# Kernel tuning notes

Measured on AMD Instinct MI355X. Metric: run time of the kernel, lower is better.

Reference implementation:

```python
import jax, jax.numpy as jnp
import numpy as np


def _ln(x, g, b, eps=1e-5):
    m = x.mean(-1, keepdims=True)
    v = ((x - m) ** 2).mean(-1, keepdims=True)
    return (x - m) * jax.lax.rsqrt(v + eps) * g + b


def setup_inputs() -> dict:
    key = jax.random.key(0)
    ks = jax.random.split(key, 16)
    B, C, D, H, W = 1, 192, 8, 32, 32
    nh, k, hid = 6, 7, 768
    n = lambda i, shape: jax.random.normal(ks[i], shape, dtype=jnp.float32) * 0.02
    return {
        'x': jax.random.normal(ks[0], (B, C, D, H, W), dtype=jnp.float32),
        'pos_emb': n(1, (1, D, C)),
        't_ln1_g': jnp.ones((C,), jnp.float32), 't_ln1_b': jnp.zeros((C,), jnp.float32),
        't_qkv_w': n(2, (C, 3 * C)),
        't_out_w': n(3, (C, C)), 't_out_b': jnp.zeros((C,), jnp.float32),
        't_ln2_g': jnp.ones((C,), jnp.float32), 't_ln2_b': jnp.zeros((C,), jnp.float32),
        't_fc1_w': n(4, (C, hid)), 't_fc1_b': jnp.zeros((hid,), jnp.float32),
        't_fc2_w': n(5, (hid, C)), 't_fc2_b': jnp.zeros((C,), jnp.float32),
        't_lnf_g': jnp.ones((C,), jnp.float32), 't_lnf_b': jnp.zeros((C,), jnp.float32),
        's_ln1_g': jnp.ones((C,), jnp.float32), 's_ln1_b': jnp.zeros((C,), jnp.float32),
        's_qkv_w': n(6, (C, 3 * C)), 's_qkv_b': jnp.zeros((3 * C,), jnp.float32),
        's_rpb': n(7, (nh, 2 * k - 1, 2 * k - 1)),
        's_proj_w': n(8, (C, C)), 's_proj_b': jnp.zeros((C,), jnp.float32),
        's_ln2_g': jnp.ones((C,), jnp.float32), 's_ln2_b': jnp.zeros((C,), jnp.float32),
        's_fc1_w': n(9, (C, hid)), 's_fc1_b': jnp.zeros((hid,), jnp.float32),
        's_fc2_w': n(10, (hid, C)), 's_fc2_b': jnp.zeros((C,), jnp.float32),
    }


def reference(x, pos_emb, t_ln1_g, t_ln1_b, t_qkv_w, t_out_w, t_out_b,
              t_ln2_g, t_ln2_b, t_fc1_w, t_fc1_b, t_fc2_w, t_fc2_b,
              t_lnf_g, t_lnf_b, s_ln1_g, s_ln1_b, s_qkv_w, s_qkv_b, s_rpb,
              s_proj_w, s_proj_b, s_ln2_g, s_ln2_b, s_fc1_w, s_fc1_b,
              s_fc2_w, s_fc2_b):
    B, C, D, H, W = x.shape
    nh = 6
    d = C // nh
    k = 7
    scale = d ** -0.5

    # ---- Time transformer: attend over the D frames per spatial position ----
    t = jnp.transpose(x, (0, 3, 4, 2, 1)).reshape(B * H * W, D, C)  # (b h w) s c
    t = t + pos_emb
    y = _ln(t, t_ln1_g, t_ln1_b)
    qkv = (y @ t_qkv_w).reshape(-1, D, 3, nh, d)
    q, kk, v = [jnp.transpose(qkv[:, :, i], (0, 2, 1, 3)) for i in range(3)]  # [N,nh,D,d]
    att = jax.nn.softmax(jnp.einsum('nhid,nhjd->nhij', q, kk) * scale, axis=-1)
    o = jnp.einsum('nhij,nhjd->nhid', att, v)
    o = jnp.transpose(o, (0, 2, 1, 3)).reshape(-1, D, C)
    t = t + (o @ t_out_w + t_out_b)
    y = _ln(t, t_ln2_g, t_ln2_b)
    t = t + (jax.nn.gelu(y @ t_fc1_w + t_fc1_b, approximate=False) @ t_fc2_w + t_fc2_b)
    t = _ln(t, t_lnf_g, t_lnf_b)
    x = x + jnp.transpose(t.reshape(B, H, W, D, C), (0, 4, 3, 1, 2))

    # ---- Space transformer: neighborhood (NAT) attention per frame ----
    s = jnp.transpose(x, (0, 2, 3, 4, 1)).reshape(B * D, H, W, C)  # (b s) h w c
    shortcut = s
    y = _ln(s, s_ln1_g, s_ln1_b)
    qkv = (y @ s_qkv_w + s_qkv_b).reshape(B * D, H, W, 3, nh, d)
    qkv = jnp.transpose(qkv, (3, 0, 4, 1, 2, 5))  # [3,N,nh,H,W,d]
    q, kk, v = qkv[0] * scale, qkv[1], qkv[2]
    half = k // 2
    sh = jnp.clip(jnp.arange(H) - half, 0, H - k)   # window start per row (edge-clamped)
    sw = jnp.clip(jnp.arange(W) - half, 0, W - k)
    idx_h = sh[:, None] + jnp.arange(k)             # [H,k] neighbor rows
    idx_w = sw[:, None] + jnp.arange(k)             # [W,k] neighbor cols
    rel_h = idx_h - jnp.arange(H)[:, None] + (k - 1)  # rel-pos-bias indices in [0,2k-2]
    rel_w = idx_w - jnp.arange(W)[:, None] + (k - 1)
    Kn = kk[:, :, idx_h][:, :, :, :, idx_w]  # [N,nh,H,k,W,k,d]
    Vn = v[:, :, idx_h][:, :, :, :, idx_w]
    att = jnp.einsum('nehwd,nehawbd->nehwab', q, Kn)  # [N,nh,H,W,k,k]
    bias = jnp.transpose(s_rpb[:, rel_h][:, :, :, rel_w], (0, 1, 3, 2, 4))  # [nh,H,W,k,k]
    att = att + bias[None]
    shp = att.shape
    att = jax.nn.softmax(att.reshape(shp[0], shp[1], shp[2], shp[3], k * k), axis=-1).reshape(shp)
    o = jnp.einsum('nehwab,nehawbd->nehwd', att, Vn)
    o = jnp.transpose(o, (0, 2, 3, 1, 4)).reshape(B * D, H, W, C)
    s = shortcut + (o @ s_proj_w + s_proj_b)
    y = _ln(s, s_ln2_g, s_ln2_b)
    s = s + (jax.nn.gelu(y @ s_fc1_w + s_fc1_b, approximate=False) @ s_fc2_w + s_fc2_b)
    x_space = jnp.transpose(s.reshape(B, D, H, W, C), (0, 4, 1, 2, 3))
    return x + x_space
```

## Files before the change

kernel.cpp:

```cpp
#include <hip/hip_runtime.h>
#include <hip/hip_bf16.h>
#include <math.h>

typedef __hip_bfloat16 bf16;
typedef short bf16x8 __attribute__((ext_vector_type(8)));
typedef float f32x4 __attribute__((ext_vector_type(4)));

__device__ __forceinline__ float b2f(bf16 v) { return __bfloat162float(v); }
__device__ __forceinline__ bf16 f2b(float v) { return __float2bfloat16(v); }
__device__ __forceinline__ float us2f(unsigned short u) {
  return __uint_as_float(((unsigned)u) << 16);
}
__device__ __forceinline__ unsigned short f2us(float f) {
  bf16 h = __float2bfloat16(f);
  return *reinterpret_cast<unsigned short*>(&h);
}
__device__ __forceinline__ float ldin(const void* p, size_t i, int f32) {
  return f32 ? ((const float*)p)[i] : b2f(((const bf16*)p)[i]);
}

#define CC 192
#define DD 8
#define HH 32
#define WW 32
#define NHEAD 6
#define HDIM 32
#define HID 768
#define NTOK 8192
#define ATT_SCALE 0.17677669529663687f

__global__ void probe_dtype_kernel(const unsigned short* __restrict__ xu,
                                   int* __restrict__ flag) {
  int lane = threadIdx.x;
  int insane = 0;
  for (int i = lane; i < 256; i += 64) {
    float a = fabsf(us2f(xu[i]));
    bool sane = (a == 0.0f) || (a > 9.5e-7f && a < 64.0f);
    if (!sane) insane++;
  }
  for (int off = 32; off; off >>= 1) insane += __shfl_xor(insane, off);
  if (lane == 0) *flag = (insane > 32) ? 1 : 0;
}

__global__ void wconv_kernel(const void* w0, const void* w1, const void* w2,
                             const void* w3, const void* w4, const void* w5,
                             const void* w6, const void* w7,
                             bf16* __restrict__ WT, const int* __restrict__ dfl) {
  int f32 = *dfl;
  int idx = blockIdx.x * 256 + threadIdx.x;
  if (idx >= 884736) return;
  const void* src; int K, N, loc;
  if      (idx < 110592) { src = w0; K = 192; N = 576; loc = idx; }
  else if (idx < 147456) { src = w1; K = 192; N = 192; loc = idx - 110592; }
  else if (idx < 294912) { src = w2; K = 192; N = 768; loc = idx - 147456; }
  else if (idx < 442368) { src = w3; K = 768; N = 192; loc = idx - 294912; }
  else if (idx < 552960) { src = w4; K = 192; N = 576; loc = idx - 442368; }
  else if (idx < 589824) { src = w5; K = 192; N = 192; loc = idx - 552960; }
  else if (idx < 737280) { src = w6; K = 192; N = 768; loc = idx - 589824; }
  else                   { src = w7; K = 768; N = 192; loc = idx - 737280; }
  int n = loc / K, k = loc - n * K;
  WT[idx] = f2b(ldin(src, (size_t)k * N + n, f32));
}

#define WOFF_TQKV  0
#define WOFF_TOUT  110592
#define WOFF_TFC1  147456
#define WOFF_TFC2  294912
#define WOFF_SQKV  442368
#define WOFF_SPROJ 552960
#define WOFF_SFC1  589824
#define WOFF_SFC2  737280

__global__ void build_ln1_kernel(const void* __restrict__ x, const void* __restrict__ pos,
                                 const void* __restrict__ g, const void* __restrict__ b,
                                 float* __restrict__ T, bf16* __restrict__ Y,
                                 const int* __restrict__ dfl) {
  int f32 = *dfl;
  int wave = (blockIdx.x * blockDim.x + threadIdx.x) >> 6;
  int lane = threadIdx.x & 63;
  if (wave >= NTOK) return;
  int d = wave & 7, hw = wave >> 3;
  float v[3];
#pragma unroll
  for (int e = 0; e < 3; e++) {
    int c = lane + e * 64;
    v[e] = ldin(x, (size_t)((c << 3) + d) * 1024 + hw, f32) +
           ldin(pos, (size_t)d * CC + c, f32);
  }
  float* tr = T + (size_t)wave * CC;
#pragma unroll
  for (int e = 0; e < 3; e++) tr[lane + e * 64] = v[e];
  float s = v[0] + v[1] + v[2];
  for (int off = 32; off; off >>= 1) s += __shfl_xor(s, off);
  float mean = s * (1.0f / CC);
  float d0 = v[0] - mean, d1 = v[1] - mean, d2 = v[2] - mean;
  float q = d0 * d0 + d1 * d1 + d2 * d2;
  for (int off = 32; off; off >>= 1) q += __shfl_xor(q, off);
  float rstd = rsqrtf(q * (1.0f / CC) + 1e-5f);
  bf16* o = Y + (size_t)wave * CC;
  o[lane]       = f2b(d0 * rstd * ldin(g, lane, f32)       + ldin(b, lane, f32));
  o[lane + 64]  = f2b(d1 * rstd * ldin(g, lane + 64, f32)  + ldin(b, lane + 64, f32));
  o[lane + 128] = f2b(d2 * rstd * ldin(g, lane + 128, f32) + ldin(b, lane + 128, f32));
}

__global__ void ln_kernel(const float* __restrict__ in, bf16* __restrict__ out,
                          const void* __restrict__ g, const void* __restrict__ b,
                          int rows, const int* __restrict__ dfl) {
  int f32 = *dfl;
  int wave = (blockIdx.x * blockDim.x + threadIdx.x) >> 6;
  int lane = threadIdx.x & 63;
  if (wave >= rows) return;
  const float* r = in + (size_t)wave * CC;
  float v0 = r[lane], v1 = r[lane + 64], v2 = r[lane + 128];
  float s = v0 + v1 + v2;
  for (int off = 32; off; off >>= 1) s += __shfl_xor(s, off);
  float mean = s * (1.0f / CC);
  float d0 = v0 - mean, d1 = v1 - mean, d2 = v2 - mean;
  float q = d0 * d0 + d1 * d1 + d2 * d2;
  for (int off = 32; off; off >>= 1) q += __shfl_xor(q, off);
  float rstd = rsqrtf(q * (1.0f / CC) + 1e-5f);
  bf16* o = out + (size_t)wave * CC;
  o[lane]       = f2b(d0 * rstd * ldin(g, lane, f32)       + ldin(b, lane, f32));
  o[lane + 64]  = f2b(d1 * rstd * ldin(g, lane + 64, f32)  + ldin(b, lane + 64, f32));
  o[lane + 128] = f2b(d2 * rstd * ldin(g, lane + 128, f32) + ldin(b, lane + 128, f32));
}

template <int TM, bool BIAS, bool GELU, bool RES, bool OUTBF, bool FINAL>
__global__ void gemm_kernel(const bf16* __restrict__ A, const bf16* __restrict__ WT,
                            const void* __restrict__ bias, const float* __restrict__ R,
                            void* __restrict__ Cout, const float* __restrict__ X2,
                            int M, int N, int K, const int* __restrict__ dfl) {
  int f32 = *dfl;
  __shared__ __align__(16) unsigned short As[TM * 64 * 72];
  __shared__ __align__(16) unsigned short Bs[64 * 72];
  int bm = blockIdx.y * (TM * 64), bn = blockIdx.x * 64;
  int tid = threadIdx.x;
  int w = tid >> 6;
  int lane = tid & 63;
  int lm = lane & 15;
  int lk = lane >> 4;

  f32x4 acc[TM][4];
#pragma unroll
  for (int i = 0; i < TM; i++)
#pragma unroll
    for (int j = 0; j < 4; j++) acc[i][j] = (f32x4){0.f, 0.f, 0.f, 0.f};

  const unsigned short* Au = reinterpret_cast<const unsigned short*>(A);
  const unsigned short* Wu = reinterpret_cast<const unsigned short*>(WT);

  for (int k0 = 0; k0 < K; k0 += 64) {
#pragma unroll
    for (int u = 0; u < TM * 2; u++) {
      int unit = tid + u * 256;
      int row = unit >> 3, seg = unit & 7;
      uint4 v = *reinterpret_cast<const uint4*>(
          &Au[(size_t)(bm + row) * K + k0 + seg * 8]);
      *reinterpret_cast<uint4*>(&As[row * 72 + seg * 8]) = v;
    }
#pragma unroll
    for (int u = 0; u < 2; u++) {
      int unit = tid + u * 256;
      int n = unit >> 3, seg = unit & 7;
      uint4 v = *reinterpret_cast<const uint4*>(
          &Wu[(size_t)(bn + n) * K + k0 + seg * 8]);
      *reinterpret_cast<uint4*>(&Bs[n * 72 + seg * 8]) = v;
    }
    __syncthreads();

#pragma unroll
    for (int kc = 0; kc < 2; kc++) {
      bf16x8 af[TM], bfr[4];
#pragma unroll
      for (int tm = 0; tm < TM; tm++)
        af[tm] = *reinterpret_cast<const bf16x8*>(
            &As[(w * (TM * 16) + tm * 16 + lm) * 72 + kc * 32 + lk * 8]);
#pragma unroll
      for (int tn = 0; tn < 4; tn++)
        bfr[tn] = *reinterpret_cast<const bf16x8*>(
            &Bs[(tn * 16 + lm) * 72 + kc * 32 + lk * 8]);
#pragma unroll
      for (int tm = 0; tm < TM; tm++)
#pragma unroll
        for (int tn = 0; tn < 4; tn++)
          acc[tm][tn] = __builtin_amdgcn_mfma_f32_16x16x32_bf16(
              af[tm], bfr[tn], acc[tm][tn], 0, 0, 0);
    }
    __syncthreads();
  }

#pragma unroll
  for (int tn = 0; tn < 4; tn++) {
    int col = bn + tn * 16 + lm;
    float bv = BIAS ? ldin(bias, col, f32) : 0.f;
#pragma unroll
    for (int tm = 0; tm < TM; tm++) {
      int row0 = bm + w * (TM * 16) + tm * 16 + lk * 4;
#pragma unroll
      for (int r = 0; r < 4; r++) {
        int row = row0 + r;
        float v = acc[tm][tn][r];
        if (BIAS) v += bv;
        if (GELU) v = 0.5f * v * (1.0f + erff(v * 0.70710678118654752f));
        size_t idx = (size_t)row * N + col;
        if (RES) v += R[idx];
        if (FINAL) {
          float o = v + X2[(size_t)row * CC + col];
          if (f32) ((float*)Cout)[(size_t)col * NTOK + row] = o;
          else     ((bf16*)Cout)[(size_t)col * NTOK + row] = f2b(o);
        } else if (OUTBF) {
          ((bf16*)Cout)[idx] = f2b(v);
        } else {
          ((float*)Cout)[idx] = v;
        }
      }
    }
  }
}

__global__ void time_attn_kernel(const bf16* __restrict__ qkv, bf16* __restrict__ O) {
  __shared__ float q[NHEAD][DD][HDIM];
  __shared__ float k[NHEAD][DD][HDIM];
  __shared__ float v[NHEAD][DD][HDIM];
  __shared__ float p[NHEAD][DD][DD];
  int n = blockIdx.x;
  int head = threadIdx.x >> 5;
  int dd = threadIdx.x & 31;
  for (int s = 0; s < DD; s++) {
    const bf16* row = qkv + (size_t)(n * DD + s) * (3 * CC);
    q[head][s][dd] = b2f(row[head * HDIM + dd]);
    k[head][s][dd] = b2f(row[CC + head * HDIM + dd]);
    v[head][s][dd] = b2f(row[2 * CC + head * HDIM + dd]);
  }
  __syncthreads();
  for (int pair = dd; pair < 64; pair += 32) {
    int sq = pair >> 3, sk = pair & 7;
    float sum = 0.f;
#pragma unroll
    for (int e = 0; e < HDIM; e++) sum += q[head][sq][e] * k[head][sk][e];
    p[head][sq][sk] = sum * ATT_SCALE;
  }
  __syncthreads();
  if (dd < DD) {
    float mx = -1e30f;
    for (int sk = 0; sk < DD; sk++) mx = fmaxf(mx, p[head][dd][sk]);
    float sum = 0.f;
    for (int sk = 0; sk < DD; sk++) { float e = expf(p[head][dd][sk] - mx); p[head][dd][sk] = e; sum += e; }
    float inv = 1.0f / sum;
    for (int sk = 0; sk < DD; sk++) p[head][dd][sk] *= inv;
  }
  __syncthreads();
  for (int sq = 0; sq < DD; sq++) {
    float sum = 0.f;
#pragma unroll
    for (int sk = 0; sk < DD; sk++) sum += p[head][sq][sk] * v[head][sk][dd];
    O[(size_t)(n * DD + sq) * CC + head * HDIM + dd] = f2b(sum);
  }
}

__global__ void epi_ln1_kernel(const float* __restrict__ T, const void* __restrict__ x,
                               const void* __restrict__ gf, const void* __restrict__ bf,
                               const void* __restrict__ g1, const void* __restrict__ b1,
                               float* __restrict__ X1T, bf16* __restrict__ Y,
                               const int* __restrict__ dfl) {
  int f32 = *dfl;
  int wave = (blockIdx.x * blockDim.x + threadIdx.x) >> 6;
  int lane = threadIdx.x & 63;
  if (wave >= NTOK) return;
  const float* r = T + (size_t)wave * CC;
  float v0 = r[lane], v1 = r[lane + 64], v2 = r[lane + 128];
  float s = v0 + v1 + v2;
  for (int off = 32; off; off >>= 1) s += __shfl_xor(s, off);
  float mean = s * (1.0f / CC);
  float d0 = v0 - mean, d1 = v1 - mean, d2 = v2 - mean;
  float q = d0 * d0 + d1 * d1 + d2 * d2;
  for (int off = 32; off; off >>= 1) q += __shfl_xor(q, off);
  float rstd = rsqrtf(q * (1.0f / CC) + 1e-5f);
  int d = wave & 7, hw = wave >> 3;
  int m = d * 1024 + hw;
  float xv[3];
#pragma unroll
  for (int e = 0; e < 3; e++) {
    int c = lane + e * 64;
    float dv = (e == 0 ? d0 : (e == 1 ? d1 : d2));
    float normed = dv * rstd * ldin(gf, c, f32) + ldin(bf, c, f32);
    xv[e] = ldin(x, (size_t)((c << 3) + d) * 1024 + hw, f32) + normed;
  }
  float* o = X1T + (size_t)m * CC;
#pragma unroll
  for (int e = 0; e < 3; e++) o[lane + e * 64] = xv[e];
  float s2 = xv[0] + xv[1] + xv[2];
  for (int off = 32; off; off >>= 1) s2 += __shfl_xor(s2, off);
  float mean2 = s2 * (1.0f / CC);
  float e0 = xv[0] - mean2, e1 = xv[1] - mean2, e2 = xv[2] - mean2;
  float q2 = e0 * e0 + e1 * e1 + e2 * e2;
  for (int off = 32; off; off >>= 1) q2 += __shfl_xor(q2, off);
  float rstd2 = rsqrtf(q2 * (1.0f / CC) + 1e-5f);
  bf16* y = Y + (size_t)m * CC;
  y[lane]       = f2b(e0 * rstd2 * ldin(g1, lane, f32)       + ldin(b1, lane, f32));
  y[lane + 64]  = f2b(e1 * rstd2 * ldin(g1, lane + 64, f32)  + ldin(b1, lane + 64, f32));
  y[lane + 128] = f2b(e2 * rstd2 * ldin(g1, lane + 128, f32) + ldin(b1, lane + 128, f32));
}

#define NKEY 224
#define PKS 40
#define PVS 232
__global__ void nat_attn_kernel(const bf16* __restrict__ qkv, const void* __restrict__ rpb,
                                bf16* __restrict__ O, const int* __restrict__ dfl) {
  int f32 = *dfl;
  __shared__ __align__(16) unsigned short Ks[NKEY * PKS];
  __shared__ __align__(16) unsigned short Vs[32 * PVS];
  __shared__ __align__(16) unsigned short Qs[64 * PKS];
  __shared__ __align__(16) unsigned short Ps[64 * PVS];
  __shared__ float rb[176];

  int blk = blockIdx.x;
  int frame = blk & 7;
  int rest = blk >> 3;
  int h = rest % 6;
  int tile = rest / 6;
  int ty = tile >> 2, tx = tile & 3;
  int base_h = min(max(ty * 8 - 3, 0), HH - 7);
  int base_w = min(max(tx * 8 - 3, 0), WW - 7);

  int tid = threadIdx.x;

  for (int i = tid; i < 169; i += 256) rb[i] = ldin(rpb, (size_t)h * 169 + i, f32);
  for (int u = tid; u < 784; u += 256) {
    int j = u >> 2, seg = u & 3;
    int a = j / 14, bb = j - a * 14;
    int ih = min(base_h + a, HH - 1), iw = min(base_w + bb, WW - 1);
    int mg = frame * 1024 + ih * 32 + iw;
    uint4 v = *reinterpret_cast<const uint4*>(qkv + (size_t)mg * 576 + 192 + h * 32 + seg * 8);
    *reinterpret_cast<uint4*>(&Ks[j * PKS + seg * 8]) = v;
  }
  for (int u = tid; u < 784; u += 256) {
    int j = u >> 2, seg = u & 3;
    int a = j / 14, bb = j - a * 14;
    int ih = min(base_h + a, HH - 1), iw = min(base_w + bb, WW - 1);
    int mg = frame * 1024 + ih * 32 + iw;
    uint4 v = *reinterpret_cast<const uint4*>(qkv + (size_t)mg * 576 + 384 + h * 32 + seg * 8);
    unsigned arr[4] = {v.x, v.y, v.z, v.w};
#pragma unroll
    for (int e = 0; e < 4; e++) {
      Vs[(seg * 8 + e * 2) * PVS + j]     = (unsigned short)(arr[e] & 0xffffu);
      Vs[(seg * 8 + e * 2 + 1) * PVS + j] = (unsigned short)(arr[e] >> 16);
    }
  }
  for (int u = tid; u < 32 * (PVS - 196); u += 256) {
    int dd = u / (PVS - 196), c = 196 + u % (PVS - 196);
    Vs[dd * PVS + c] = 0;
  }
  {
    int q = tid >> 2, seg = tid & 3;
    int qy = ty * 8 + (q >> 3), qx = tx * 8 + (q & 7);
    int mg = frame * 1024 + qy * 32 + qx;
    uint4 v = *reinterpret_cast<const uint4*>(qkv + (size_t)mg * 576 + h * 32 + seg * 8);
    *reinterpret_cast<uint4*>(&Qs[q * PKS + seg * 8]) = v;
  }
  __syncthreads();

  int w = tid >> 6;
  int lane = tid & 63;
  int c = lane & 15;
  int lk = lane >> 4;

  bf16x8 aq = *reinterpret_cast<const bf16x8*>(&Qs[(w * 16 + c) * PKS + lk * 8]);
  f32x4 sc[14];
#pragma unroll
  for (int f = 0; f < 14; f++) {
    bf16x8 bk = *reinterpret_cast<const bf16x8*>(&Ks[(f * 16 + c) * PKS + lk * 8]);
    sc[f] = __builtin_amdgcn_mfma_f32_16x16x32_bf16(aq, bk, (f32x4){0.f, 0.f, 0.f, 0.f}, 0, 0, 0);
  }

#pragma unroll
  for (int f = 0; f < 14; f++) {
    int key = f * 16 + c;
    int a = key / 14, bb = key - a * 14;
    int ih = base_h + a, iw = base_w + bb;
    bool keyok = key < 196;
#pragma unroll
    for (int r = 0; r < 4; r++) {
      int qloc = w * 16 + lk * 4 + r;
      int qy = ty * 8 + (qloc >> 3), qx = tx * 8 + (qloc & 7);
      int sh = min(max(qy - 3, 0), HH - 7);
      int sw = min(max(qx - 3, 0), WW - 7);
      bool valid = keyok && ((unsigned)(ih - sh) < 7u) && ((unsigned)(iw - sw) < 7u);
      int bidx = valid ? (ih - qy + 6) * 13 + (iw - qx + 6) : 0;
      float s = sc[f][r] * ATT_SCALE + rb[bidx];
      sc[f][r] = valid ? s : -1e30f;
    }
  }

  float sm[4];
#pragma unroll
  for (int r = 0; r < 4; r++) {
    float m = sc[0][r];
#pragma unroll
    for (int f = 1; f < 14; f++) m = fmaxf(m, sc[f][r]);
    for (int off = 8; off; off >>= 1) m = fmaxf(m, __shfl_xor(m, off));
    float s = 0.f;
#pragma unroll
    for (int f = 0; f < 14; f++) { float e = __expf(sc[f][r] - m); sc[f][r] = e; s += e; }
    for (int off = 8; off; off >>= 1) s += __shfl_xor(s, off);
    sm[r] = 1.0f / s;
  }
#pragma unroll
  for (int f = 0; f < 14; f++)
#pragma unroll
    for (int r = 0; r < 4; r++)
      Ps[(w * 16 + lk * 4 + r) * PVS + f * 16 + c] = f2us(sc[f][r] * sm[r]);
  __syncthreads();

  f32x4 oacc[2] = {(f32x4){0.f, 0.f, 0.f, 0.f}, (f32x4){0.f, 0.f, 0.f, 0.f}};
#pragma unroll
  for (int kt = 0; kt < 7; kt++) {
    bf16x8 ap = *reinterpret_cast<const bf16x8*>(&Ps[(w * 16 + c) * PVS + kt * 32 + lk * 8]);
#pragma unroll
    for (int dt = 0; dt < 2; dt++) {
      bf16x8 bv = *reinterpret_cast<const bf16x8*>(&Vs[(dt * 16 + c) * PVS + kt * 32 + lk * 8]);
      oacc[dt] = __builtin_amdgcn_mfma_f32_16x16x32_bf16(ap, bv, oacc[dt], 0, 0, 0);
    }
  }

#pragma unroll
  for (int dt = 0; dt < 2; dt++)
#pragma unroll
    for (int r = 0; r < 4; r++) {
      int qloc = w * 16 + lk * 4 + r;
      int qy = ty * 8 + (qloc >> 3), qx = tx * 8 + (qloc & 7);
      int mg = frame * 1024 + qy * 32 + qx;
      O[(size_t)mg * CC + h * 32 + dt * 16 + c] = f2b(oacc[dt][r]);
    }
}

extern "C" void kernel_launch(void* const* d_in, const int* in_sizes, int n_in,
                              void* d_out, int out_size, void* d_ws, size_t ws_size,
                              hipStream_t stream) {
  const void* x        = d_in[0];
  const void* pos_emb  = d_in[1];
  const void* t_ln1_g  = d_in[2];
  const void* t_ln1_b  = d_in[3];
  const void* t_qkv_w  = d_in[4];
  const void* t_out_w  = d_in[5];
  const void* t_out_b  = d_in[6];
  const void* t_ln2_g  = d_in[7];
  const void* t_ln2_b  = d_in[8];
  const void* t_fc1_w  = d_in[9];
  const void* t_fc1_b  = d_in[10];
  const void* t_fc2_w  = d_in[11];
  const void* t_fc2_b  = d_in[12];
  const void* t_lnf_g  = d_in[13];
  const void* t_lnf_b  = d_in[14];
  const void* s_ln1_g  = d_in[15];
  const void* s_ln1_b  = d_in[16];
  const void* s_qkv_w  = d_in[17];
  const void* s_qkv_b  = d_in[18];
  const void* s_rpb    = d_in[19];
  const void* s_proj_w = d_in[20];
  const void* s_proj_b = d_in[21];
  const void* s_ln2_g  = d_in[22];
  const void* s_ln2_b  = d_in[23];
  const void* s_fc1_w  = d_in[24];
  const void* s_fc1_b  = d_in[25];
  const void* s_fc2_w  = d_in[26];
  const void* s_fc2_b  = d_in[27];

  float* ws = (float*)d_ws;
  const size_t SZ = (size_t)NTOK * CC;
  const size_t need = (5 * SZ + 4 + 442368 + 16) * sizeof(float);
  if (ws_size < need) return;

  float* T   = ws;
  float* X1T = ws + SZ;
  bf16*  Y   = (bf16*)(ws + 2 * SZ);
  bf16*  O   = (bf16*)(ws + 2 * SZ + SZ / 2);
  bf16*  QKV = (bf16*)(ws + 3 * SZ);
  bf16*  Hb  = QKV;
  float* S   = T;
  int*   dfl = (int*)(ws + 5 * SZ);
  bf16*  WT  = (bf16*)(ws + 5 * SZ + 4);

  dim3 blk256(256);

  probe_dtype_kernel<<<1, 64, 0, stream>>>((const unsigned short*)x, dfl);
  wconv_kernel<<<3456, blk256, 0, stream>>>(
      t_qkv_w, t_out_w, t_fc1_w, t_fc2_w, s_qkv_w, s_proj_w, s_fc1_w, s_fc2_w, WT, dfl);

  build_ln1_kernel<<<NTOK / 4, blk256, 0, stream>>>(x, pos_emb, t_ln1_g, t_ln1_b, T, Y, dfl);
  gemm_kernel<2, false, false, false, true, false><<<dim3(9, 64), blk256, 0, stream>>>(
      Y, WT + WOFF_TQKV, nullptr, nullptr, QKV, nullptr, NTOK, 3 * CC, CC, dfl);
  time_attn_kernel<<<1024, 192, 0, stream>>>(QKV, O);
  gemm_kernel<1, true, false, true, false, false><<<dim3(3, 128), blk256, 0, stream>>>(
      O, WT + WOFF_TOUT, t_out_b, T, T, nullptr, NTOK, CC, CC, dfl);
  ln_kernel<<<NTOK / 4, blk256, 0, stream>>>(T, Y, t_ln2_g, t_ln2_b, NTOK, dfl);
  gemm_kernel<2, true, true, false, true, false><<<dim3(12, 64), blk256, 0, stream>>>(
      Y, WT + WOFF_TFC1, t_fc1_b, nullptr, Hb, nullptr, NTOK, HID, CC, dfl);
  gemm_kernel<1, true, false, true, false, false><<<dim3(3, 128), blk256, 0, stream>>>(
      Hb, WT + WOFF_TFC2, t_fc2_b, T, T, nullptr, NTOK, CC, HID, dfl);
  epi_ln1_kernel<<<NTOK / 4, blk256, 0, stream>>>(
      T, x, t_lnf_g, t_lnf_b, s_ln1_g, s_ln1_b, X1T, Y, dfl);

  gemm_kernel<2, true, false, false, true, false><<<dim3(9, 64), blk256, 0, stream>>>(
      Y, WT + WOFF_SQKV, s_qkv_b, nullptr, QKV, nullptr, NTOK, 3 * CC, CC, dfl);
  nat_attn_kernel<<<768, blk256, 0, stream>>>(QKV, s_rpb, O, dfl);
  gemm_kernel<1, true, false, true, false, false><<<dim3(3, 128), blk256, 0, stream>>>(
      O, WT + WOFF_SPROJ, s_proj_b, X1T, S, nullptr, NTOK, CC, CC, dfl);
  ln_kernel<<<NTOK / 4, blk256, 0, stream>>>(S, Y, s_ln2_g, s_ln2_b, NTOK, dfl);
  gemm_kernel<2, true, true, false, true, false><<<dim3(12, 64), blk256, 0, stream>>>(
      Y, WT + WOFF_SFC1, s_fc1_b, nullptr, Hb, nullptr, NTOK, HID, CC, dfl);
  gemm_kernel<1, true, false, true, false, true><<<dim3(3, 128), blk256, 0, stream>>>(
      Hb, WT + WOFF_SFC2, s_fc2_b, S, d_out, X1T, NTOK, CC, HID, dfl);
}
```

Baseline: 279.7 us.

## Fuse N=192 GEMMs with following LayerNorm and merge dtype probe into weight conversion

```diff
diff --git a/kernel.cpp b/kernel.cpp
--- a/kernel.cpp
+++ b/kernel.cpp
@@ -29,24 +29,22 @@
 #define NTOK 8192
 #define ATT_SCALE 0.17677669529663687f
 
-__global__ void probe_dtype_kernel(const unsigned short* __restrict__ xu,
-                                   int* __restrict__ flag) {
-  int lane = threadIdx.x;
-  int insane = 0;
-  for (int i = lane; i < 256; i += 64) {
-    float a = fabsf(us2f(xu[i]));
-    bool sane = (a == 0.0f) || (a > 9.5e-7f && a < 64.0f);
-    if (!sane) insane++;
-  }
-  for (int off = 32; off; off >>= 1) insane += __shfl_xor(insane, off);
-  if (lane == 0) *flag = (insane > 32) ? 1 : 0;
-}
-
-__global__ void wconv_kernel(const void* w0, const void* w1, const void* w2,
+__global__ void wconv_kernel(const unsigned short* __restrict__ xu,
+                             const void* w0, const void* w1, const void* w2,
                              const void* w3, const void* w4, const void* w5,
                              const void* w6, const void* w7,
-                             bf16* __restrict__ WT, const int* __restrict__ dfl) {
-  int f32 = *dfl;
+                             bf16* __restrict__ WT, int* __restrict__ flag) {
+  __shared__ int cnt[4];
+  {
+    float a = fabsf(us2f(xu[threadIdx.x]));
+    bool insane = !((a == 0.0f) || (a > 9.5e-7f && a < 64.0f));
+    unsigned long long mask = __ballot(insane);
+    if ((threadIdx.x & 63) == 0) cnt[threadIdx.x >> 6] = __popcll(mask);
+  }
+  __syncthreads();
+  int f32 = (cnt[0] + cnt[1] + cnt[2] + cnt[3]) > 32;
+  if (blockIdx.x == 0 && threadIdx.x == 0) *flag = f32;
+
   int idx = blockIdx.x * 256 + threadIdx.x;
   if (idx >= 884736) return;
   const void* src; int K, N, loc;
@@ -98,28 +96,6 @@
   for (int off = 32; off; off >>= 1) q += __shfl_xor(q, off);
   float rstd = rsqrtf(q * (1.0f / CC) + 1e-5f);
   bf16* o = Y + (size_t)wave * CC;
-  o[lane]       = f2b(d0 * rstd * ldin(g, lane, f32)       + ldin(b, lane, f32));
-  o[lane + 64]  = f2b(d1 * rstd * ldin(g, lane + 64, f32)  + ldin(b, lane + 64, f32));
-  o[lane + 128] = f2b(d2 * rstd * ldin(g, lane + 128, f32) + ldin(b, lane + 128, f32));
-}
-
-__global__ void ln_kernel(const float* __restrict__ in, bf16* __restrict__ out,
-                          const void* __restrict__ g, const void* __restrict__ b,
-                          int rows, const int* __restrict__ dfl) {
-  int f32 = *dfl;
-  int wave = (blockIdx.x * blockDim.x + threadIdx.x) >> 6;
-  int lane = threadIdx.x & 63;
-  if (wave >= rows) return;
-  const float* r = in + (size_t)wave * CC;
-  float v0 = r[lane], v1 = r[lane + 64], v2 = r[lane + 128];
-  float s = v0 + v1 + v2;
-  for (int off = 32; off; off >>= 1) s += __shfl_xor(s, off);
-  float mean = s * (1.0f / CC);
-  float d0 = v0 - mean, d1 = v1 - mean, d2 = v2 - mean;
-  float q = d0 * d0 + d1 * d1 + d2 * d2;
-  for (int off = 32; off; off >>= 1) q += __shfl_xor(q, off);
-  float rstd = rsqrtf(q * (1.0f / CC) + 1e-5f);
-  bf16* o = out + (size_t)wave * CC;
   o[lane]       = f2b(d0 * rstd * ldin(g, lane, f32)       + ldin(b, lane, f32));
   o[lane + 64]  = f2b(d1 * rstd * ldin(g, lane + 64, f32)  + ldin(b, lane + 64, f32));
   o[lane + 128] = f2b(d2 * rstd * ldin(g, lane + 128, f32) + ldin(b, lane + 128, f32));
@@ -218,6 +194,126 @@
   }
 }
 
+template <bool EPI>
+__global__ void gemm_ln_kernel(const bf16* __restrict__ A, const bf16* __restrict__ WT,
+                               const void* __restrict__ bias, const float* __restrict__ R,
+                               const void* __restrict__ x,
+                               const void* __restrict__ g0, const void* __restrict__ b0,
+                               const void* __restrict__ g1, const void* __restrict__ b1,
+                               float* __restrict__ Fout, bf16* __restrict__ Yout,
+                               int K, const int* __restrict__ dfl) {
+  int f32 = *dfl;
+  __shared__ __align__(16) unsigned short As[64 * 72];
+  __shared__ __align__(16) unsigned short Bs[192 * 72];
+  int bm = blockIdx.x * 64;
+  int tid = threadIdx.x;
+  int w = tid >> 6;
+  int lane = tid & 63;
+  int lm = lane & 15;
+  int lk = lane >> 4;
+
+  f32x4 acc[12];
+#pragma unroll
+  for (int j = 0; j < 12; j++) acc[j] = (f32x4){0.f, 0.f, 0.f, 0.f};
+
+  const unsigned short* Au = reinterpret_cast<const unsigned short*>(A);
+  const unsigned short* Wu = reinterpret_cast<const unsigned short*>(WT);
+
+  for (int k0 = 0; k0 < K; k0 += 64) {
+#pragma unroll
+    for (int u = 0; u < 2; u++) {
+      int unit = tid + u * 256;
+      int row = unit >> 3, seg = unit & 7;
+      uint4 v = *reinterpret_cast<const uint4*>(
+          &Au[(size_t)(bm + row) * K + k0 + seg * 8]);
+      *reinterpret_cast<uint4*>(&As[row * 72 + seg * 8]) = v;
+    }
+#pragma unroll
+    for (int u = 0; u < 6; u++) {
+      int unit = tid + u * 256;
+      int n = unit >> 3, seg = unit & 7;
+      uint4 v = *reinterpret_cast<const uint4*>(
+          &Wu[(size_t)n * K + k0 + seg * 8]);
+      *reinterpret_cast<uint4*>(&Bs[n * 72 + seg * 8]) = v;
+    }
+    __syncthreads();
+
+#pragma unroll
+    for (int kc = 0; kc < 2; kc++) {
+      bf16x8 af = *reinterpret_cast<const bf16x8*>(
+          &As[(w * 16 + lm) * 72 + kc * 32 + lk * 8]);
+#pragma unroll
+      for (int tn = 0; tn < 12; tn++) {
+        bf16x8 bfr = *reinterpret_cast<const bf16x8*>(
+            &Bs[(tn * 16 + lm) * 72 + kc * 32 + lk * 8]);
+        acc[tn] = __builtin_amdgcn_mfma_f32_16x16x32_bf16(af, bfr, acc[tn], 0, 0, 0);
+      }
+    }
+    __syncthreads();
+  }
+
+  float bv[12];
+#pragma unroll
+  for (int tn = 0; tn < 12; tn++) bv[tn] = ldin(bias, tn * 16 + lm, f32);
+
+#pragma unroll
+  for (int r = 0; r < 4; r++) {
+    int row = bm + w * 16 + lk * 4 + r;
+    float v[12];
+    float s = 0.f;
+#pragma unroll
+    for (int tn = 0; tn < 12; tn++) {
+      float t = acc[tn][r] + bv[tn] + R[(size_t)row * CC + tn * 16 + lm];
+      v[tn] = t;
+      s += t;
+    }
+    for (int off = 1; off < 16; off <<= 1) s += __shfl_xor(s, off);
+    float mean = s * (1.0f / CC);
+    float q = 0.f;
+#pragma unroll
+    for (int tn = 0; tn < 12; tn++) { float d = v[tn] - mean; q += d * d; }
+    for (int off = 1; off < 16; off <<= 1) q += __shfl_xor(q, off);
+    float rstd = rsqrtf(q * (1.0f / CC) + 1e-5f);
+
+    if (!EPI) {
+#pragma unroll
+      for (int tn = 0; tn < 12; tn++) {
+        int col = tn * 16 + lm;
+        Fout[(size_t)row * CC + col] = v[tn];
+        Yout[(size_t)row * CC + col] =
+            f2b((v[tn] - mean) * rstd * ldin(g0, col, f32) + ldin(b0, col, f32));
+      }
+    } else {
+      int d = row & 7, hw = row >> 3;
+      int m = d * 1024 + hw;
+      float xv[12];
+      float s2 = 0.f;
+#pragma unroll
+      for (int tn = 0; tn < 12; tn++) {
+        int col = tn * 16 + lm;
+        float normed = (v[tn] - mean) * rstd * ldin(g0, col, f32) + ldin(b0, col, f32);
+        float t = ldin(x, (size_t)((col << 3) + d) * 1024 + hw, f32) + normed;
+        xv[tn] = t;
+        s2 += t;
+        Fout[(size_t)m * CC + col] = t;
+      }
+      for (int off = 1; off < 16; off <<= 1) s2 += __shfl_xor(s2, off);
+      float mean2 = s2 * (1.0f / CC);
+      float q2 = 0.f;
+#pragma unroll
+      for (int tn = 0; tn < 12; tn++) { float dd = xv[tn] - mean2; q2 += dd * dd; }
+      for (int off = 1; off < 16; off <<= 1) q2 += __shfl_xor(q2, off);
+      float rstd2 = rsqrtf(q2 * (1.0f / CC) + 1e-5f);
+#pragma unroll
+      for (int tn = 0; tn < 12; tn++) {
+        int col = tn * 16 + lm;
+        Yout[(size_t)m * CC + col] =
+            f2b((xv[tn] - mean2) * rstd2 * ldin(g1, col, f32) + ldin(b1, col, f32));
+      }
+    }
+  }
+}
+
 __global__ void time_attn_kernel(const bf16* __restrict__ qkv, bf16* __restrict__ O) {
   __shared__ float q[NHEAD][DD][HDIM];
   __shared__ float k[NHEAD][DD][HDIM];
@@ -256,50 +352,6 @@
     for (int sk = 0; sk < DD; sk++) sum += p[head][sq][sk] * v[head][sk][dd];
     O[(size_t)(n * DD + sq) * CC + head * HDIM + dd] = f2b(sum);
   }
-}
-
-__global__ void epi_ln1_kernel(const float* __restrict__ T, const void* __restrict__ x,
-                               const void* __restrict__ gf, const void* __restrict__ bf,
-                               const void* __restrict__ g1, const void* __restrict__ b1,
-                               float* __restrict__ X1T, bf16* __restrict__ Y,
-                               const int* __restrict__ dfl) {
-  int f32 = *dfl;
-  int wave = (blockIdx.x * blockDim.x + threadIdx.x) >> 6;
-  int lane = threadIdx.x & 63;
-  if (wave >= NTOK) return;
-  const float* r = T + (size_t)wave * CC;
-  float v0 = r[lane], v1 = r[lane + 64], v2 = r[lane + 128];
-  float s = v0 + v1 + v2;
-  for (int off = 32; off; off >>= 1) s += __shfl_xor(s, off);
-  float mean = s * (1.0f / CC);
-  float d0 = v0 - mean, d1 = v1 - mean, d2 = v2 - mean;
-  float q = d0 * d0 + d1 * d1 + d2 * d2;
-  for (int off = 32; off; off >>= 1) q += __shfl_xor(q, off);
-  float rstd = rsqrtf(q * (1.0f / CC) + 1e-5f);
-  int d = wave & 7, hw = wave >> 3;
-  int m = d * 1024 + hw;
-  float xv[3];
-#pragma unroll
-  for (int e = 0; e < 3; e++) {
-    int c = lane + e * 64;
-    float dv = (e == 0 ? d0 : (e == 1 ? d1 : d2));
-    float normed = dv * rstd * ldin(gf, c, f32) + ldin(bf, c, f32);
-    xv[e] = ldin(x, (size_t)((c << 3) + d) * 1024 + hw, f32) + normed;
-  }
-  float* o = X1T + (size_t)m * CC;
-#pragma unroll
-  for (int e = 0; e < 3; e++) o[lane + e * 64] = xv[e];
-  float s2 = xv[0] + xv[1] + xv[2];
-  for (int off = 32; off; off >>= 1) s2 += __shfl_xor(s2, off);
-  float mean2 = s2 * (1.0f / CC);
-  float e0 = xv[0] - mean2, e1 = xv[1] - mean2, e2 = xv[2] - mean2;
-  float q2 = e0 * e0 + e1 * e1 + e2 * e2;
-  for (int off = 32; off; off >>= 1) q2 += __shfl_xor(q2, off);
-  float rstd2 = rsqrtf(q2 * (1.0f / CC) + 1e-5f);
-  bf16* y = Y + (size_t)m * CC;
-  y[lane]       = f2b(e0 * rstd2 * ldin(g1, lane, f32)       + ldin(b1, lane, f32));
-  y[lane + 64]  = f2b(e1 * rstd2 * ldin(g1, lane + 64, f32)  + ldin(b1, lane + 64, f32));
-  y[lane + 128] = f2b(e2 * rstd2 * ldin(g1, lane + 128, f32) + ldin(b1, lane + 128, f32));
 }
 
 #define NKEY 224
@@ -483,30 +535,29 @@
 
   dim3 blk256(256);
 
-  probe_dtype_kernel<<<1, 64, 0, stream>>>((const unsigned short*)x, dfl);
   wconv_kernel<<<3456, blk256, 0, stream>>>(
+      (const unsigned short*)x,
       t_qkv_w, t_out_w, t_fc1_w, t_fc2_w, s_qkv_w, s_proj_w, s_fc1_w, s_fc2_w, WT, dfl);
 
   build_ln1_kernel<<<NTOK / 4, blk256, 0, stream>>>(x, pos_emb, t_ln1_g, t_ln1_b, T, Y, dfl);
   gemm_kernel<2, false, false, false, true, false><<<dim3(9, 64), blk256, 0, stream>>>(
       Y, WT + WOFF_TQKV, nullptr, nullptr, QKV, nullptr, NTOK, 3 * CC, CC, dfl);
   time_attn_kernel<<<1024, 192, 0, stream>>>(QKV, O);
-  gemm_kernel<1, true, false, true, false, false><<<dim3(3, 128), blk256, 0, stream>>>(
-      O, WT + WOFF_TOUT, t_out_b, T, T, nullptr, NTOK, CC, CC, dfl);
-  ln_kernel<<<NTOK / 4, blk256, 0, stream>>>(T, Y, t_ln2_g, t_ln2_b, NTOK, dfl);
+  gemm_ln_kernel<false><<<128, blk256, 0, stream>>>(
+      O, WT + WOFF_TOUT, t_out_b, T, nullptr, t_ln2_g, t_ln2_b, nullptr, nullptr,
+      T, Y, CC, dfl);
   gemm_kernel<2, true, true, false, true, false><<<dim3(12, 64), blk256, 0, stream>>>(
       Y, WT + WOFF_TFC1, t_fc1_b, nullptr, Hb, nullptr, NTOK, HID, CC, dfl);
-  gemm_kernel<1, true, false, true, false, false><<<dim3(3, 128), blk256, 0, stream>>>(
-      Hb, WT + WOFF_TFC2, t_fc2_b, T, T, nullptr, NTOK, CC, HID, dfl);
-  epi_ln1_kernel<<<NTOK / 4, blk256, 0, stream>>>(
-      T, x, t_lnf_g, t_lnf_b, s_ln1_g, s_ln1_b, X1T, Y, dfl);
+  gemm_ln_kernel<true><<<128, blk256, 0, stream>>>(
+      Hb, WT + WOFF_TFC2, t_fc2_b, T, x, t_lnf_g, t_lnf_b, s_ln1_g, s_ln1_b,
+      X1T, Y, HID, dfl);
 
   gemm_kernel<2, true, false, false, true, false><<<dim3(9, 64), blk256, 0, stream>>>(
       Y, WT + WOFF_SQKV, s_qkv_b, nullptr, QKV, nullptr, NTOK, 3 * CC, CC, dfl);
   nat_attn_kernel<<<768, blk256, 0, stream>>>(QKV, s_rpb, O, dfl);
-  gemm_kernel<1, true, false, true, false, false><<<dim3(3, 128), blk256, 0, stream>>>(
-      O, WT + WOFF_SPROJ, s_proj_b, X1T, S, nullptr, NTOK, CC, CC, dfl);
-  ln_kernel<<<NTOK / 4, blk256, 0, stream>>>(S, Y, s_ln2_g, s_ln2_b, NTOK, dfl);
+  gemm_ln_kernel<false><<<128, blk256, 0, stream>>>(
+      O, WT + WOFF_SPROJ, s_proj_b, X1T, nullptr, s_ln2_g, s_ln2_b, nullptr, nullptr,
+      S, Y, CC, dfl);
   gemm_kernel<2, true, true, false, true, false><<<dim3(12, 64), blk256, 0, stream>>>(
       Y, WT + WOFF_SFC1, s_fc1_b, nullptr, Hb, nullptr, NTOK, HID, CC, dfl);
   gemm_kernel<1, true, false, true, false, true><<<dim3(3, 128), blk256, 0, stream>>>(
```

After: 326.6 us. 16.8% more time.

## Fuse LayerNorm into FC1 GEMM prologue and fold dtype probe into weight conversion

Applied to the files above, without the earlier changes.

```diff
diff --git a/kernel.cpp b/kernel.cpp
--- a/kernel.cpp
+++ b/kernel.cpp
@@ -29,24 +29,22 @@
 #define NTOK 8192
 #define ATT_SCALE 0.17677669529663687f
 
-__global__ void probe_dtype_kernel(const unsigned short* __restrict__ xu,
-                                   int* __restrict__ flag) {
-  int lane = threadIdx.x;
-  int insane = 0;
-  for (int i = lane; i < 256; i += 64) {
-    float a = fabsf(us2f(xu[i]));
-    bool sane = (a == 0.0f) || (a > 9.5e-7f && a < 64.0f);
-    if (!sane) insane++;
-  }
-  for (int off = 32; off; off >>= 1) insane += __shfl_xor(insane, off);
-  if (lane == 0) *flag = (insane > 32) ? 1 : 0;
-}
-
-__global__ void wconv_kernel(const void* w0, const void* w1, const void* w2,
+__global__ void wconv_kernel(const unsigned short* __restrict__ xu,
+                             const void* w0, const void* w1, const void* w2,
                              const void* w3, const void* w4, const void* w5,
                              const void* w6, const void* w7,
-                             bf16* __restrict__ WT, const int* __restrict__ dfl) {
-  int f32 = *dfl;
+                             bf16* __restrict__ WT, int* __restrict__ flag) {
+  __shared__ int cnt[4];
+  {
+    float a = fabsf(us2f(xu[threadIdx.x]));
+    bool insane = !((a == 0.0f) || (a > 9.5e-7f && a < 64.0f));
+    unsigned long long mask = __ballot(insane);
+    if ((threadIdx.x & 63) == 0) cnt[threadIdx.x >> 6] = __popcll(mask);
+  }
+  __syncthreads();
+  int f32 = (cnt[0] + cnt[1] + cnt[2] + cnt[3]) > 32;
+  if (blockIdx.x == 0 && threadIdx.x == 0) *flag = f32;
+
   int idx = blockIdx.x * 256 + threadIdx.x;
   if (idx >= 884736) return;
   const void* src; int K, N, loc;
@@ -98,28 +96,6 @@
   for (int off = 32; off; off >>= 1) q += __shfl_xor(q, off);
   float rstd = rsqrtf(q * (1.0f / CC) + 1e-5f);
   bf16* o = Y + (size_t)wave * CC;
-  o[lane]       = f2b(d0 * rstd * ldin(g, lane, f32)       + ldin(b, lane, f32));
-  o[lane + 64]  = f2b(d1 * rstd * ldin(g, lane + 64, f32)  + ldin(b, lane + 64, f32));
-  o[lane + 128] = f2b(d2 * rstd * ldin(g, lane + 128, f32) + ldin(b, lane + 128, f32));
-}
-
-__global__ void ln_kernel(const float* __restrict__ in, bf16* __restrict__ out,
-                          const void* __restrict__ g, const void* __restrict__ b,
-                          int rows, const int* __restrict__ dfl) {
-  int f32 = *dfl;
-  int wave = (blockIdx.x * blockDim.x + threadIdx.x) >> 6;
-  int lane = threadIdx.x & 63;
-  if (wave >= rows) return;
-  const float* r = in + (size_t)wave * CC;
-  float v0 = r[lane], v1 = r[lane + 64], v2 = r[lane + 128];
-  float s = v0 + v1 + v2;
-  for (int off = 32; off; off >>= 1) s += __shfl_xor(s, off);
-  float mean = s * (1.0f / CC);
-  float d0 = v0 - mean, d1 = v1 - mean, d2 = v2 - mean;
-  float q = d0 * d0 + d1 * d1 + d2 * d2;
-  for (int off = 32; off; off >>= 1) q += __shfl_xor(q, off);
-  float rstd = rsqrtf(q * (1.0f / CC) + 1e-5f);
-  bf16* o = out + (size_t)wave * CC;
   o[lane]       = f2b(d0 * rstd * ldin(g, lane, f32)       + ldin(b, lane, f32));
   o[lane + 64]  = f2b(d1 * rstd * ldin(g, lane + 64, f32)  + ldin(b, lane + 64, f32));
   o[lane + 128] = f2b(d2 * rstd * ldin(g, lane + 128, f32) + ldin(b, lane + 128, f32));
@@ -213,6 +189,114 @@
         } else {
           ((float*)Cout)[idx] = v;
         }
+      }
+    }
+  }
+}
+
+#define FSTR 200
+__global__ void gemm_fc1ln_kernel(const float* __restrict__ A, const bf16* __restrict__ WT,
+                                  const void* __restrict__ g, const void* __restrict__ b,
+                                  const void* __restrict__ bias,
+                                  bf16* __restrict__ Hb, const int* __restrict__ dfl) {
+  int f32 = *dfl;
+  __shared__ __align__(16) unsigned short As[128 * FSTR];
+  __shared__ __align__(16) unsigned short Bs[64 * FSTR];
+  __shared__ float gb[384];
+  int bm = blockIdx.y * 128, bn = blockIdx.x * 64;
+  int tid = threadIdx.x;
+
+  for (int i = tid; i < 384; i += 256)
+    gb[i] = (i < 192) ? ldin(g, i, f32) : ldin(b, i - 192, f32);
+  const unsigned short* Wu = reinterpret_cast<const unsigned short*>(WT);
+#pragma unroll
+  for (int u = 0; u < 6; u++) {
+    int unit = tid + u * 256;
+    int n = unit / 24, seg = unit - n * 24;
+    uint4 v = *reinterpret_cast<const uint4*>(&Wu[(size_t)(bn + n) * 192 + seg * 8]);
+    *reinterpret_cast<uint4*>(&Bs[n * FSTR + seg * 8]) = v;
+  }
+  __syncthreads();
+
+#pragma unroll
+  for (int p = 0; p < 2; p++) {
+    int rowloc = p * 64 + (tid >> 2);
+    int q = tid & 3;
+    const float* ar = A + (size_t)(bm + rowloc) * 192 + q * 48;
+    float v[48];
+    float s = 0.f;
+#pragma unroll
+    for (int i = 0; i < 12; i++) {
+      float4 f4 = *reinterpret_cast<const float4*>(ar + i * 4);
+      v[i * 4] = f4.x; v[i * 4 + 1] = f4.y; v[i * 4 + 2] = f4.z; v[i * 4 + 3] = f4.w;
+      s += f4.x + f4.y + f4.z + f4.w;
+    }
+    s += __shfl_xor(s, 1); s += __shfl_xor(s, 2);
+    float mean = s * (1.0f / 192.0f);
+    float qv = 0.f;
+#pragma unroll
+    for (int i = 0; i < 48; i++) { float d = v[i] - mean; qv += d * d; }
+    qv += __shfl_xor(qv, 1); qv += __shfl_xor(qv, 2);
+    float rstd = rsqrtf(qv * (1.0f / 192.0f) + 1e-5f);
+#pragma unroll
+    for (int i = 0; i < 6; i++) {
+      uint4 pk;
+      unsigned* pu = reinterpret_cast<unsigned*>(&pk);
+#pragma unroll
+      for (int e = 0; e < 4; e++) {
+        int i0 = i * 8 + e * 2;
+        int c0 = q * 48 + i0;
+        unsigned lo = f2us((v[i0]     - mean) * rstd * gb[c0]     + gb[192 + c0]);
+        unsigned hi = f2us((v[i0 + 1] - mean) * rstd * gb[c0 + 1] + gb[192 + c0 + 1]);
+        pu[e] = lo | (hi << 16);
+      }
+      *reinterpret_cast<uint4*>(&As[rowloc * FSTR + q * 48 + i * 8]) = pk;
+    }
+  }
+  __syncthreads();
+
+  int w = tid >> 6;
+  int lane = tid & 63;
+  int lm = lane & 15;
+  int lk = lane >> 4;
+
+  f32x4 acc[2][4];
+#pragma unroll
+  for (int i = 0; i < 2; i++)
+#pragma unroll
+    for (int j = 0; j < 4; j++) acc[i][j] = (f32x4){0.f, 0.f, 0.f, 0.f};
+
+#pragma unroll
+  for (int kc = 0; kc < 6; kc++) {
+    bf16x8 af[2], bfr[4];
+#pragma unroll
+    for (int tm = 0; tm < 2; tm++)
+      af[tm] = *reinterpret_cast<const bf16x8*>(
+          &As[(w * 32 + tm * 16 + lm) * FSTR + kc * 32 + lk * 8]);
+#pragma unroll
+    for (int tn = 0; tn < 4; tn++)
+      bfr[tn] = *reinterpret_cast<const bf16x8*>(
+          &Bs[(tn * 16 + lm) * FSTR + kc * 32 + lk * 8]);
+#pragma unroll
+    for (int tm = 0; tm < 2; tm++)
+#pragma unroll
+      for (int tn = 0; tn < 4; tn++)
+        acc[tm][tn] = __builtin_amdgcn_mfma_f32_16x16x32_bf16(
+            af[tm], bfr[tn], acc[tm][tn], 0, 0, 0);
+  }
+
+#pragma unroll
+  for (int tn = 0; tn < 4; tn++) {
+    int col = bn + tn * 16 + lm;
+    float bv = ldin(bias, col, f32);
+#pragma unroll
+    for (int tm = 0; tm < 2; tm++) {
+      int row0 = bm + w * 32 + tm * 16 + lk * 4;
+#pragma unroll
+      for (int r = 0; r < 4; r++) {
+        float v = acc[tm][tn][r] + bv;
+        v = 0.5f * v * (1.0f + erff(v * 0.70710678118654752f));
+        Hb[(size_t)(row0 + r) * HID + col] = f2b(v);
       }
     }
   }
@@ -483,8 +567,8 @@
 
   dim3 blk256(256);
 
-  probe_dtype_kernel<<<1, 64, 0, stream>>>((const unsigned short*)x, dfl);
   wconv_kernel<<<3456, blk256, 0, stream>>>(
+      (const unsigned short*)x,
       t_qkv_w, t_out_w, t_fc1_w, t_fc2_w, s_qkv_w, s_proj_w, s_fc1_w, s_fc2_w, WT, dfl);
 
   build_ln1_kernel<<<NTOK / 4, blk256, 0, stream>>>(x, pos_emb, t_ln1_g, t_ln1_b, T, Y, dfl);
@@ -493,9 +577,8 @@
   time_attn_kernel<<<1024, 192, 0, stream>>>(QKV, O);
   gemm_kernel<1, true, false, true, false, false><<<dim3(3, 128), blk256, 0, stream>>>(
       O, WT + WOFF_TOUT, t_out_b, T, T, nullptr, NTOK, CC, CC, dfl);
-  ln_kernel<<<NTOK / 4, blk256, 0, stream>>>(T, Y, t_ln2_g, t_ln2_b, NTOK, dfl);
-  gemm_kernel<2, true, true, false, true, false><<<dim3(12, 64), blk256, 0, stream>>>(
-      Y, WT + WOFF_TFC1, t_fc1_b, nullptr, Hb, nullptr, NTOK, HID, CC, dfl);
+  gemm_fc1ln_kernel<<<dim3(12, 64), blk256, 0, stream>>>(
+      T, WT + WOFF_TFC1, t_ln2_g, t_ln2_b, t_fc1_b, Hb, dfl);
   gemm_kernel<1, true, false, true, false, false><<<dim3(3, 128), blk256, 0, stream>>>(
       Hb, WT + WOFF_TFC2, t_fc2_b, T, T, nullptr, NTOK, CC, HID, dfl);
   epi_ln1_kernel<<<NTOK / 4, blk256, 0, stream>>>(
@@ -506,9 +589,8 @@
   nat_attn_kernel<<<768, blk256, 0, stream>>>(QKV, s_rpb, O, dfl);
   gemm_kernel<1, true, false, true, false, false><<<dim3(3, 128), blk256, 0, stream>>>(
       O, WT + WOFF_SPROJ, s_proj_b, X1T, S, nullptr, NTOK, CC, CC, dfl);
-  ln_kernel<<<NTOK / 4, blk256, 0, stream>>>(S, Y, s_ln2_g, s_ln2_b, NTOK, dfl);
-  gemm_kernel<2, true, true, false, true, false><<<dim3(12, 64), blk256, 0, stream>>>(
-      Y, WT + WOFF_SFC1, s_fc1_b, nullptr, Hb, nullptr, NTOK, HID, CC, dfl);
+  gemm_fc1ln_kernel<<<dim3(12, 64), blk256, 0, stream>>>(
+      S, WT + WOFF_SFC1, s_ln2_g, s_ln2_b, s_fc1_b, Hb, dfl);
   gemm_kernel<1, true, false, true, false, true><<<dim3(3, 128), blk256, 0, stream>>>(
       Hb, WT + WOFF_SFC2, s_fc2_b, S, d_out, X1T, NTOK, CC, HID, dfl);
 }
```

After: 311.9 us. 1.12x slower.
